# Kernel optimization log

Measured on AMD Instinct MI355X. Metric: run time of the kernel, lower is better.

Reference implementation:

```python
import jax, jax.numpy as jnp
import numpy as np

B, NP, DIM = 32, 1369, 768
NCLS, K = 200, 5
C = NCLS + 1          # n_classes + background
H = W = 37            # sqrt(NP)
GAMMA = 0.99
SCALE = 4.0
SINKHORN_ITERS = 3
PCA_ITERS = 10
PCA_THRESH = 0.5
EPS = 1e-8


def _l2norm(x):
    return x / jnp.clip(jnp.linalg.norm(x, axis=-1, keepdims=True), EPS)


def setup_inputs() -> dict:
    key = jax.random.key(0)
    k1, k2, k3 = jax.random.split(key, 3)
    patch_tokens = jax.random.normal(k1, (B, NP, DIM), dtype=jnp.float32)
    labels = jax.random.randint(k2, (B,), 0, NCLS)
    prototypes = 0.02 * jax.random.normal(k3, (C, K, DIM), dtype=jnp.float32)  # trunc_normal std=0.02 approx
    sa = jnp.full((NCLS, K), 0.5, dtype=jnp.float32)
    scale = jnp.asarray(SCALE, dtype=jnp.float32)
    return {"patch_tokens": patch_tokens, "labels": labels,
            "prototypes": prototypes, "sa": sa, "scale": scale}


def reference(patch_tokens, labels, prototypes, sa, scale):
    # --- cosine patch-prototype similarity ---
    tok_n = _l2norm(patch_tokens)                 # [B, NP, D]
    pro_n = _l2norm(prototypes)                   # [C, K, D]
    logits = scale * jnp.einsum('bnd,ckd->bnck', tok_n, pro_n)  # [B, NP, C, K]

    # --- avg pooling + 'sa' classification head ---
    image_logits = logits.mean(axis=1)            # [B, C, K]
    sa_w = jax.nn.softmax(sa, axis=-1) * K        # [NCLS, K]
    class_logits = (image_logits[:, :NCLS, :] * sa_w).sum(axis=-1)  # [B, NCLS]

    # --- PCA pseudo patch labels (power iteration, q=1, centered) ---
    X = jax.lax.stop_gradient(patch_tokens).reshape(-1, DIM)  # [N, D]
    Xc = X - X.mean(axis=0, keepdims=True)
    v = jax.random.normal(jax.random.key(42), (DIM,), dtype=jnp.float32)
    for _ in range(PCA_ITERS):
        u = Xc @ v
        v = Xc.T @ u
        v = v / jnp.clip(jnp.linalg.norm(v), EPS)
    u = Xc @ v
    U = u / jnp.clip(jnp.linalg.norm(u), EPS)     # leading left singular vector
    U_scaled = (U - U.min()) / jnp.clip(U.max() - U.min(), EPS)
    U_img = U_scaled.reshape(B, H, W)
    pseudo = jnp.where(U_img <= PCA_THRESH,
                       labels[:, None, None],
                       C - 1).astype(jnp.int32)   # [B, H, W]

    # --- online clustering: masked sinkhorn vectorized over classes ---
    flat_lab = pseudo.reshape(-1)                 # [N]
    cls_ids = jnp.arange(C)
    mask = (flat_lab[:, None] == cls_ids[None, :]).astype(jnp.float32)  # [N, C]
    Nc = mask.sum(axis=0)                         # [C] fg patch count per class
    Lf = jax.lax.stop_gradient(logits).reshape(-1, C, K)
    Q = jnp.exp(Lf) * mask[:, :, None]            # [N, C, K], zero outside class mask
    Q = Q / jnp.clip(Q.sum(axis=(0, 2)), EPS)[None, :, None]
    Ncc = jnp.clip(Nc, 1.0)
    for _ in range(SINKHORN_ITERS):
        Q = Q / jnp.clip(Q.sum(axis=0), EPS)[None] / K           # col normalize
        Q = Q / jnp.clip(Q.sum(axis=2, keepdims=True), EPS) / Ncc[None, :, None]  # row normalize
    Q = Q * Nc[None, :, None]
    tok_flat = jax.lax.stop_gradient(tok_n).reshape(-1, DIM)
    P_new = jnp.einsum('nck,nd->ckd', Q, tok_flat)               # [C, K, D]
    updated = GAMMA * prototypes + (1.0 - GAMMA) * P_new          # momentum update
    present = jnp.isin(cls_ids, labels)                           # classes in this batch
    new_prototypes = jnp.where(present[:, None, None], updated, prototypes)

    return (logits, image_logits, class_logits, pseudo, new_prototypes)
```

## Files before the change

### kernel.cpp

```cpp
#include <hip/hip_runtime.h>

constexpr int   BB    = 32;
constexpr int   NPP   = 1369;
constexpr int   DIMC  = 768;
constexpr int   NCLSC = 200;
constexpr int   KP    = 5;
constexpr int   CC    = 201;
constexpr int   CKC   = 1005;
constexpr int   NPAD  = 1024;
constexpr int   NTOK  = BB * NPP;
constexpr float EPSF  = 1e-8f;
constexpr int   PWIN  = 128;
constexpr int   MTILES = 343;
constexpr int   LDK   = 40;

typedef __attribute__((ext_vector_type(8))) short bf16x8;
typedef __attribute__((ext_vector_type(4))) float f32x4;

constexpr size_t O_LOG = 0;
constexpr size_t O_IMG = (size_t)NTOK * CKC;
constexpr size_t O_CLS = O_IMG + (size_t)BB * CKC;
constexpr size_t O_PSE = O_CLS + (size_t)BB * NCLSC;
constexpr size_t O_PRO = O_PSE + (size_t)NTOK;

constexpr size_t W_PRONBF = 0;
constexpr size_t W_INVN   = W_PRONBF + (size_t)NPAD*DIMC/2;
constexpr size_t W_MU     = W_INVN + NTOK;
constexpr size_t W_COLS   = W_MU + 2*DIMC;
constexpr size_t W_VBUF   = W_COLS + 2*DIMC;
constexpr size_t W_SSUM   = W_VBUF + 2*11*DIMC;
constexpr size_t W_TSUM   = W_SSUM + 32;
constexpr size_t W_NC     = W_TSUM + CC;
constexpr size_t W_FILL   = W_NC + CC;
constexpr size_t W_PRES   = W_FILL + CC;
constexpr size_t ZG_LEN   = (W_PRES + CC) - W_COLS;
constexpr size_t W_CSQ    = W_PRES + CC;
constexpr size_t W_U      = ((W_CSQ + CKC) + 1) & ~(size_t)1;
constexpr size_t W_PART   = W_U + 2*NTOK;
constexpr size_t W_SCAL   = W_PART + 2*1536;
constexpr size_t W_Q      = W_SCAL + 16;
constexpr size_t W_PNEW   = W_Q + (size_t)NTOK*KP;
constexpr size_t W_PLAB   = W_PNEW + (size_t)CC*KP*DIMC;
constexpr size_t W_OFFS   = W_PLAB + NTOK;
constexpr size_t W_RLST   = W_OFFS + 256;
constexpr size_t W_XBF    = ((W_RLST + NTOK) + 3) & ~(size_t)3;
constexpr size_t W_END_BIG  = W_XBF + (size_t)(NTOK + 128)*DIMC/2;
constexpr size_t W_PRON32   = W_XBF;
constexpr size_t W_END_FALL = W_PRON32 + (size_t)CKC*DIMC;

__device__ __forceinline__ unsigned short f2bf(float x) {
    unsigned u = __float_as_uint(x);
    unsigned r = (u + 0x7fffu + ((u >> 16) & 1u)) >> 16;
    return (unsigned short)r;
}

__global__ void fill_zero(float* p, int n) {
    int i = blockIdx.x * 256 + threadIdx.x;
    if (i < n) p[i] = 0.0f;
}

__global__ __launch_bounds__(256) void tok_stats(const float* __restrict__ X,
                                                 float* __restrict__ invn,
                                                 double* __restrict__ colsD,
                                                 unsigned short* __restrict__ xbf) {
    const int lane = threadIdx.x & 63;
    const int gw   = blockIdx.x * 4 + (threadIdx.x >> 6);
    double cacc[12];
    #pragma unroll
    for (int j = 0; j < 12; j++) cacc[j] = 0.0;
    for (int n = gw; n < NTOK; n += 1024) {
        const float* row = X + (size_t)n * DIMC;
        float s = 0.0f;
        float x[12];
        #pragma unroll
        for (int j = 0; j < 12; j++) {
            x[j] = row[lane + 64*j];
            s = fmaf(x[j], x[j], s);
            cacc[j] += (double)x[j];
        }
        if (xbf) {
            unsigned short* orow = xbf + (size_t)n * DIMC;
            #pragma unroll
            for (int j = 0; j < 12; j++) orow[lane + 64*j] = f2bf(x[j]);
        }
        #pragma unroll
        for (int o = 32; o >= 1; o >>= 1) s += __shfl_xor(s, o);
        if (lane == 0) invn[n] = 1.0f / fmaxf(sqrtf(s), EPSF);
    }
    #pragma unroll
    for (int j = 0; j < 12; j++) atomicAdd(&colsD[lane + 64*j], cacc[j]);
}

__global__ __launch_bounds__(256) void proto_norm(const float* __restrict__ P,
                                                  unsigned short* __restrict__ pbf,
                                                  float* __restrict__ p32) {
    const int lane = threadIdx.x & 63;
    const int gw   = blockIdx.x * 4 + (threadIdx.x >> 6);
    for (int j = gw; j < NPAD; j += 256) {
        unsigned short* obf = pbf + (size_t)j * DIMC;
        if (j >= CKC) {
            #pragma unroll
            for (int t = 0; t < 12; t++) obf[lane + 64*t] = 0;
            continue;
        }
        const float* row = P + (size_t)j * DIMC;
        float x[12]; float s = 0.0f;
        #pragma unroll
        for (int t = 0; t < 12; t++) { x[t] = row[lane + 64*t]; s = fmaf(x[t], x[t], s); }
        #pragma unroll
        for (int o = 32; o >= 1; o >>= 1) s += __shfl_xor(s, o);
        float nrm = fmaxf(sqrtf(s), EPSF);
        #pragma unroll
        for (int t = 0; t < 12; t++) {
            float nv = x[t] / nrm;
            obf[lane + 64*t] = f2bf(nv);
            if (p32) p32[(size_t)j * DIMC + lane + 64*t] = nv;
        }
    }
}

__global__ __launch_bounds__(256) void logits_gemm(
        const unsigned short* __restrict__ Xbf,
        const unsigned short* __restrict__ Pbf,
        const float* __restrict__ invn,
        const float* __restrict__ scale_p,
        float* __restrict__ out,
        float* __restrict__ img) {
    __shared__ unsigned short As[128 * LDK];
    __shared__ unsigned short Bs[128 * LDK];
    const int b   = blockIdx.x;
    const int swz = (b & 7) * MTILES + (b >> 3);
    const int row_t = swz >> 3, col_t = swz & 7;
    const int row0 = row_t * 128, col0 = col_t * 128;
    const int tid = threadIdx.x, lane = tid & 63, wid = tid >> 6;
    const int wm = (wid >> 1) * 64, wn = (wid & 1) * 64;
    const int fr = lane & 15, fq = lane >> 4;

    f32x4 acc[4][4] = {};

    const int srow = tid >> 1, sk = (tid & 1) * 16;
    const unsigned short* aSrc = Xbf + (size_t)(row0 + srow) * DIMC + sk;
    const unsigned short* bSrc = Pbf + (size_t)(col0 + srow) * DIMC + sk;
    unsigned short* aDst = As + srow * LDK + sk;
    unsigned short* bDst = Bs + srow * LDK + sk;

    for (int ks = 0; ks < DIMC / 32; ks++) {
        bf16x8 a0 = *(const bf16x8*)(aSrc + ks * 32);
        bf16x8 a1 = *(const bf16x8*)(aSrc + ks * 32 + 8);
        bf16x8 b0 = *(const bf16x8*)(bSrc + ks * 32);
        bf16x8 b1 = *(const bf16x8*)(bSrc + ks * 32 + 8);
        __syncthreads();
        *(bf16x8*)(aDst)     = a0; *(bf16x8*)(aDst + 8) = a1;
        *(bf16x8*)(bDst)     = b0; *(bf16x8*)(bDst + 8) = b1;
        __syncthreads();
        bf16x8 af[4], bfr[4];
        #pragma unroll
        for (int m = 0; m < 4; m++)
            af[m] = *(const bf16x8*)(As + (wm + m * 16 + fr) * LDK + fq * 8);
        #pragma unroll
        for (int n = 0; n < 4; n++)
            bfr[n] = *(const bf16x8*)(Bs + (wn + n * 16 + fr) * LDK + fq * 8);
        #pragma unroll
        for (int m = 0; m < 4; m++)
            #pragma unroll
            for (int n = 0; n < 4; n++)
                acc[m][n] = __builtin_amdgcn_mfma_f32_16x16x32_bf16(af[m], bfr[n], acc[m][n], 0, 0, 0);
    }

    const float sc = *scale_p;
    #pragma unroll
    for (int m = 0; m < 4; m++) {
        const int rbase = row0 + wm + m * 16 + fq * 4;
        float fin[4];
        #pragma unroll
        for (int rr = 0; rr < 4; rr++) {
            int rrow = rbase + rr;
            fin[rr] = (rrow < NTOK) ? sc * invn[rrow] : 0.0f;
        }
        const int strip0 = row0 + wm + m * 16;
        const bool sameImg = ((strip0 / NPP) == ((strip0 + 15) / NPP)) && (strip0 + 15) < NTOK;
        const int bimg = strip0 / NPP;
        #pragma unroll
        for (int n = 0; n < 4; n++) {
            const int col = col0 + wn + n * 16 + fr;
            const bool cok = col < CKC;
            float csum = 0.0f;
            #pragma unroll
            for (int rr = 0; rr < 4; rr++) {
                int rrow = rbase + rr;
                float v = fin[rr] * acc[m][n][rr];
                if (cok && rrow < NTOK) out[(size_t)rrow * CKC + col] = v;
                csum += v;
            }
            if (sameImg) {
                csum += __shfl_xor(csum, 16);
                csum += __shfl_xor(csum, 32);
                if (lane < 16 && cok) atomicAdd(&img[bimg * CKC + col], csum);
            } else if (cok) {
                #pragma unroll
                for (int rr = 0; rr < 4; rr++) {
                    int rrow = rbase + rr;
                    if (rrow < NTOK)
                        atomicAdd(&img[(rrow / NPP) * CKC + col], fin[rr] * acc[m][n][rr]);
                }
            }
        }
    }
}

__global__ __launch_bounds__(256) void gemm_logits(const float* __restrict__ X,
                                                   const float* __restrict__ Bn,
                                                   const float* __restrict__ invn,
                                                   const float* __restrict__ scale_p,
                                                   float* __restrict__ out) {
    __shared__ float As[32][68];
    __shared__ float Bs[32][68];
    const int tid = threadIdx.x;
    const int tx = tid & 15, ty = tid >> 4;
    const int row0 = blockIdx.x * 64;
    const int col0 = blockIdx.y * 64;
    const int lm = tid >> 2;
    const int kb = (tid & 3) * 8;
    float acc[4][4] = {};
    for (int k0 = 0; k0 < DIMC; k0 += 32) {
        float a[8], b[8];
        int ar = row0 + lm;
        if (ar < NTOK) {
            const float* ap = X + (size_t)ar * DIMC + k0 + kb;
            #pragma unroll
            for (int j = 0; j < 8; j++) a[j] = ap[j];
        } else {
            #pragma unroll
            for (int j = 0; j < 8; j++) a[j] = 0.0f;
        }
        int bc = col0 + lm;
        if (bc < CKC) {
            const float* bp = Bn + (size_t)bc * DIMC + k0 + kb;
            #pragma unroll
            for (int j = 0; j < 8; j++) b[j] = bp[j];
        } else {
            #pragma unroll
            for (int j = 0; j < 8; j++) b[j] = 0.0f;
        }
        __syncthreads();
        #pragma unroll
        for (int j = 0; j < 8; j++) As[kb + j][lm] = a[j];
        #pragma unroll
        for (int j = 0; j < 8; j++) Bs[kb + j][lm] = b[j];
        __syncthreads();
        #pragma unroll
        for (int kk = 0; kk < 32; kk++) {
            float av[4], bv[4];
            #pragma unroll
            for (int i = 0; i < 4; i++) av[i] = As[kk][ty*4 + i];
            #pragma unroll
            for (int j = 0; j < 4; j++) bv[j] = Bs[kk][tx*4 + j];
            #pragma unroll
            for (int i = 0; i < 4; i++)
                #pragma unroll
                for (int j = 0; j < 4; j++)
                    acc[i][j] = fmaf(av[i], bv[j], acc[i][j]);
        }
    }
    const float sc = *scale_p;
    #pragma unroll
    for (int i = 0; i < 4; i++) {
        int r = row0 + ty*4 + i;
        if (r >= NTOK) continue;
        float f = sc * invn[r];
        float* orow = out + (size_t)r * CKC;
        #pragma unroll
        for (int j = 0; j < 4; j++) {
            int c = col0 + tx*4 + j;
            if (c < CKC) orow[c] = f * acc[i][j];
        }
    }
}

__global__ void img_reduce(const float* __restrict__ logits, float* __restrict__ img) {
    int b = blockIdx.x, jc = blockIdx.y, nc = blockIdx.z;
    int j = jc * 256 + threadIdx.x;
    if (j >= CKC) return;
    int p0 = nc * 172, p1 = min(NPP, p0 + 172);
    const float* base = logits + (size_t)b * NPP * CKC + j;
    float s = 0.0f;
    for (int p = p0; p < p1; p++) s += base[(size_t)p * CKC];
    atomicAdd(&img[b * CKC + j], s);
}

__global__ __launch_bounds__(256) void img_final(float* __restrict__ img,
                                                 const float* __restrict__ sa,
                                                 float* __restrict__ cls) {
    int b = blockIdx.x;
    for (int i = threadIdx.x; i < CKC; i += 256)
        img[b * CKC + i] = img[b * CKC + i] / 1369.0f;
    __syncthreads();
    for (int c = threadIdx.x; c < NCLSC; c += 256) {
        float vv[KP]; float mx = -3.4e38f;
        #pragma unroll
        for (int k = 0; k < KP; k++) { vv[k] = sa[c * KP + k]; mx = fmaxf(mx, vv[k]); }
        float e[KP]; float s = 0.0f;
        #pragma unroll
        for (int k = 0; k < KP; k++) { e[k] = expf(vv[k] - mx); s += e[k]; }
        float cl = 0.0f;
        #pragma unroll
        for (int k = 0; k < KP; k++) {
            float sw = e[k] / s * 5.0f;
            cl += img[b * CKC + c * KP + k] * sw;
        }
        cls[b * NCLSC + c] = cl;
    }
}

__global__ void mu_final(const double* __restrict__ colsD, double* __restrict__ mu) {
    int d = threadIdx.x;
    mu[d] = colsD[d] / (double)NTOK;
}

__device__ __forceinline__ float bits_to_normal(unsigned bits) {
    float f = __uint_as_float((bits >> 9) | 0x3f800000u) - 1.0f;
    const float lo = -0.99999994f;
    float u = f * 2.0f + lo;
    u = fmaxf(lo, u);
    float w = -log1pf(-u * u);
    float p;
    if (w < 5.0f) {
        w -= 2.5f;
        p = 2.81022636e-08f;
        p = fmaf(p, w, 3.43273939e-07f);
        p = fmaf(p, w, -3.5233877e-06f);
        p = fmaf(p, w, -4.39150654e-06f);
        p = fmaf(p, w, 0.00021858087f);
        p = fmaf(p, w, -0.00125372503f);
        p = fmaf(p, w, -0.00417768164f);
        p = fmaf(p, w, 0.246640727f);
        p = fmaf(p, w, 1.50140941f);
    } else {
        w = sqrtf(w) - 3.0f;
        p = -0.000200214257f;
        p = fmaf(p, w, 0.000100950558f);
        p = fmaf(p, w, 0.00134934322f);
        p = fmaf(p, w, -0.00367342844f);
        p = fmaf(p, w, 0.00573950773f);
        p = fmaf(p, w, -0.0076224613f);
        p = fmaf(p, w, 0.00943887047f);
        p = fmaf(p, w, 1.00167406f);
        p = fmaf(p, w, 2.83297682f);
    }
    return 1.41421356237f * (p * u);
}

#define TF_ROUND(r) { x0 += x1; x1 = (x1 << r) | (x1 >> (32 - r)); x1 ^= x0; }
__global__ void v0_gen(double* __restrict__ v) {
    int i = blockIdx.x * 256 + threadIdx.x;
    if (i >= DIMC) return;
    unsigned x0 = 0u, x1 = (unsigned)i;
    const unsigned k0 = 0u, k1 = 42u, k2 = k0 ^ k1 ^ 0x1BD11BDAu;
    x0 += k0; x1 += k1;
    TF_ROUND(13) TF_ROUND(15) TF_ROUND(26) TF_ROUND(6)
    x0 += k1; x1 += k2 + 1u;
    TF_ROUND(17) TF_ROUND(29) TF_ROUND(16) TF_ROUND(24)
    x0 += k2; x1 += k0 + 2u;
    TF_ROUND(13) TF_ROUND(15) TF_ROUND(26) TF_ROUND(6)
    x0 += k0; x1 += k1 + 3u;
    TF_ROUND(17) TF_ROUND(29) TF_ROUND(16) TF_ROUND(24)
    x0 += k1; x1 += k2 + 4u;
    TF_ROUND(13) TF_ROUND(15) TF_ROUND(26) TF_ROUND(6)
    x0 += k2; x1 += k0 + 5u;
    v[i] = (double)bits_to_normal(x0 ^ x1);
}

__global__ __launch_bounds__(256) void pca_pass(const float* __restrict__ X,
                                                const double* __restrict__ mu,
                                                const double* __restrict__ vraw,
                                                const double* __restrict__ Sin,
                                                double* __restrict__ vnext,
                                                double* __restrict__ Snext) {
    __shared__ double ve[768];
    __shared__ double red[256];
    __shared__ double wacc[4][768];
    const int tid = threadIdx.x, lane = tid & 63, wid = tid >> 6;
    const double S = *Sin;
    double mv = 0.0;
    for (int c = tid; c < 768; c += 256) {
        double x = vraw[c] - S * mu[c];
        ve[c] = x;
        mv += mu[c] * x;
    }
    red[tid] = mv; __syncthreads();
    for (int s = 128; s > 0; s >>= 1) { if (tid < s) red[tid] += red[tid + s]; __syncthreads(); }
    const double muv = red[0];
    for (int c = tid; c < 4 * 768; c += 256) ((double*)wacc)[c] = 0.0;
    __syncthreads();
    double acc[12] = {};
    double usum = 0.0;
    for (int n = blockIdx.x * 4 + wid; n < NTOK; n += 2048) {
        const float* row = X + (size_t)n * DIMC;
        float x[12];
        double s = 0.0;
        #pragma unroll
        for (int j = 0; j < 12; j++) {
            x[j] = row[lane + 64*j];
            s = fma((double)x[j], ve[lane + 64*j], s);
        }
        #pragma unroll
        for (int o = 32; o >= 1; o >>= 1) s += __shfl_xor(s, o);
        double uu = s - muv;
        usum += uu;
        #pragma unroll
        for (int j = 0; j < 12; j++) acc[j] = fma((double)x[j], uu, acc[j]);
    }
    #pragma unroll
    for (int j = 0; j < 12; j++) wacc[wid][lane + 64*j] = acc[j];
    if (lane == 0) red[wid] = usum;
    __syncthreads();
    for (int c = tid; c < 768; c += 256)
        atomicAdd(&vnext[c], wacc[0][c] + wacc[1][c] + wacc[2][c] + wacc[3][c]);
    if (tid == 0) atomicAdd(Snext, red[0] + red[1] + red[2] + red[3]);
}

__global__ __launch_bounds__(256) void u_final(const float* __restrict__ X,
                                               const double* __restrict__ mu,
                                               const double* __restrict__ vraw,
                                               const double* __restrict__ Sin,
                                               double* __restrict__ u,
                                               double* __restrict__ part) {
    __shared__ double ve[768];
    __shared__ double red[256];
    __shared__ double wmin[4], wmax[4], wss[4];
    const int tid = threadIdx.x, lane = tid & 63, wid = tid >> 6;
    const double S = *Sin;
    double mv = 0.0;
    for (int c = tid; c < 768; c += 256) {
        double x = vraw[c] - S * mu[c];
        ve[c] = x;
        mv += mu[c] * x;
    }
    red[tid] = mv; __syncthreads();
    for (int s = 128; s > 0; s >>= 1) { if (tid < s) red[tid] += red[tid + s]; __syncthreads(); }
    const double muv = red[0];
    double lmin = 1e300, lmax = -1e300, lss = 0.0;
    for (int n = blockIdx.x * 4 + wid; n < NTOK; n += 2048) {
        const float* row = X + (size_t)n * DIMC;
        double s = 0.0;
        #pragma unroll
        for (int j = 0; j < 12; j++) s = fma((double)row[lane + 64*j], ve[lane + 64*j], s);
        #pragma unroll
        for (int o = 32; o >= 1; o >>= 1) s += __shfl_xor(s, o);
        double uu = s - muv;
        if (lane == 0) {
            u[n] = uu;
            lmin = fmin(lmin, uu); lmax = fmax(lmax, uu); lss = fma(uu, uu, lss);
        }
    }
    if (lane == 0) { wmin[wid] = lmin; wmax[wid] = lmax; wss[wid] = lss; }
    __syncthreads();
    if (tid == 0) {
        part[blockIdx.x]        = fmin(fmin(wmin[0], wmin[1]), fmin(wmin[2], wmin[3]));
        part[512 + blockIdx.x]  = fmax(fmax(wmax[0], wmax[1]), fmax(wmax[2], wmax[3]));
        part[1024 + blockIdx.x] = wss[0] + wss[1] + wss[2] + wss[3];
    }
}

__global__ __launch_bounds__(512) void final_scalars(const double* __restrict__ part,
                                                     double* __restrict__ scal,
                                                     const int* __restrict__ labels,
                                                     int* __restrict__ pres) {
    __shared__ double rmin[512], rmax[512], rss[512];
    int t = threadIdx.x;
    rmin[t] = part[t]; rmax[t] = part[512 + t]; rss[t] = part[1024 + t];
    __syncthreads();
    for (int s = 256; s > 0; s >>= 1) {
        if (t < s) {
            rmin[t] = fmin(rmin[t], rmin[t + s]);
            rmax[t] = fmax(rmax[t], rmax[t + s]);
            rss[t] += rss[t + s];
        }
        __syncthreads();
    }
    if (t == 0) {
        double nrm = fmax(sqrt(rss[0]), 1e-8);
        double Umin = rmin[0] / nrm;
        double Umax = rmax[0] / nrm;
        scal[1] = nrm;
        scal[2] = Umin;
        scal[3] = fmax(Umax - Umin, 1e-8);
    }
    if (t < BB) pres[labels[t]] = 1;
}

__global__ __launch_bounds__(256) void pseudo_kernel(
        const double* __restrict__ u, const double* __restrict__ scal,
        const int* __restrict__ labels, float* __restrict__ pse,
        int* __restrict__ plab, int* __restrict__ Nc) {
    __shared__ int hist[CC];
    const int tid = threadIdx.x;
    for (int c = tid; c < CC; c += 256) hist[c] = 0;
    __syncthreads();
    int n = blockIdx.x * 256 + tid;
    if (n < NTOK) {
        double U  = u[n] / scal[1];
        double Us = (U - scal[2]) / scal[3];
        int lab = (Us <= 0.5) ? labels[n / NPP] : (CC - 1);
        pse[n] = (float)lab;
        plab[n] = lab;
        atomicAdd(&hist[lab], 1);
    }
    __syncthreads();
    for (int c = tid; c < CC; c += 256)
        if (hist[c] > 0) atomicAdd(&Nc[c], hist[c]);
}

__global__ void offs_scan(const int* __restrict__ Nc, int* __restrict__ offs) {
    if (threadIdx.x == 0) {
        int s = 0;
        for (int c = 0; c < CC; c++) { offs[c] = s; s += Nc[c]; }
        offs[CC] = s;
    }
}

__global__ __launch_bounds__(256) void scatter_rows(
        const int* __restrict__ plab, const int* __restrict__ offs,
        int* __restrict__ fill, int* __restrict__ rlist) {
    __shared__ int hist[CC];
    __shared__ int base[CC];
    const int tid = threadIdx.x;
    for (int c = tid; c < CC; c += 256) hist[c] = 0;
    __syncthreads();
    int n = blockIdx.x * 256 + tid;
    int lab = -1, posl = 0;
    if (n < NTOK) {
        lab = plab[n];
        posl = atomicAdd(&hist[lab], 1);
    }
    __syncthreads();
    for (int c = tid; c < CC; c += 256) {
        int h = hist[c];
        if (h > 0) base[c] = atomicAdd(&fill[c], h);
    }
    __syncthreads();
    if (n < NTOK) rlist[offs[lab] + base[lab] + posl] = n;
}

__global__ __launch_bounds__(256) void sinkhorn_fused(
        const float* __restrict__ logits,
        const int* __restrict__ offs,
        const int* __restrict__ rlist,
        float* __restrict__ qseg) {
    const int c  = blockIdx.x;
    const int i0 = offs[c], i1 = offs[c + 1];
    const int cnt = i1 - i0;
    if (cnt <= 0) return;
    const int tid = threadIdx.x;
    __shared__ float cs[KP];
    __shared__ float redk[KP][4];

    for (int i = i0 + tid; i < i1; i += 256) {
        int n = rlist[i];
        const float* lp = logits + (size_t)n * CKC + c * KP;
        #pragma unroll
        for (int k = 0; k < KP; k++) qseg[(size_t)i * KP + k] = expf(lp[k]);
    }
    const float Ncc = fmaxf((float)cnt, 1.0f);
    for (int it = 0; it < 3; it++) {
        __syncthreads();
        float lc[KP] = {};
        for (int i = i0 + tid; i < i1; i += 256) {
            #pragma unroll
            for (int k = 0; k < KP; k++) lc[k] += qseg[(size_t)i * KP + k];
        }
        #pragma unroll
        for (int k = 0; k < KP; k++) {
            float v = lc[k];
            #pragma unroll
            for (int o = 32; o >= 1; o >>= 1) v += __shfl_xor(v, o);
            if ((tid & 63) == 0) redk[k][tid >> 6] = v;
        }
        __syncthreads();
        if (tid == 0) {
            #pragma unroll
            for (int k = 0; k < KP; k++)
                cs[k] = fmaxf(redk[k][0] + redk[k][1] + redk[k][2] + redk[k][3], EPSF) * 5.0f;
        }
        __syncthreads();
        float inv_cs[KP];
        #pragma unroll
        for (int k = 0; k < KP; k++) inv_cs[k] = 1.0f / cs[k];
        const float outsc = (it == 2) ? ((float)cnt / Ncc) : (1.0f / Ncc);
        for (int i = i0 + tid; i < i1; i += 256) {
            float v[KP]; float rs = 0.0f;
            #pragma unroll
            for (int k = 0; k < KP; k++) { v[k] = qseg[(size_t)i*KP + k] * inv_cs[k]; rs += v[k]; }
            float f = outsc / fmaxf(rs, EPSF);
            #pragma unroll
            for (int k = 0; k < KP; k++) qseg[(size_t)i*KP + k] = v[k] * f;
        }
    }
}

__global__ __launch_bounds__(256) void pnew_partial(
        const float* __restrict__ X,
        const float* __restrict__ invn,
        const float* __restrict__ qseg,
        const int* __restrict__ offs,
        const int* __restrict__ rlist,
        const int* __restrict__ plab,
        float* __restrict__ Pnew) {
    const int d = blockIdx.y * 256 + threadIdx.x;
    const int fgEnd = offs[CC - 1];
    int i0 = blockIdx.x * PWIN;
    if (i0 >= fgEnd) return;
    int i1 = min(i0 + PWIN, fgEnd);
    int curlab = -1;
    float acc[KP] = {};
    for (int i = i0; i < i1; i++) {
        int n = rlist[i];
        int lab = plab[n];
        if (lab != curlab) {
            if (curlab >= 0) {
                #pragma unroll
                for (int k = 0; k < KP; k++)
                    atomicAdd(&Pnew[((size_t)curlab * KP + k) * DIMC + d], acc[k]);
            }
            curlab = lab;
            #pragma unroll
            for (int k = 0; k < KP; k++) acc[k] = 0.0f;
        }
        float x = X[(size_t)n * DIMC + d] * invn[n];
        #pragma unroll
        for (int k = 0; k < KP; k++) acc[k] = fmaf(qseg[(size_t)i * KP + k], x, acc[k]);
    }
    if (curlab >= 0) {
        #pragma unroll
        for (int k = 0; k < KP; k++)
            atomicAdd(&Pnew[((size_t)curlab * KP + k) * DIMC + d], acc[k]);
    }
}

__global__ void proto_out(const float* __restrict__ proto, const float* __restrict__ Pnew,
                          const int* __restrict__ pres, float* __restrict__ outp) {
    int idx = blockIdx.x * 256 + threadIdx.x;
    if (idx >= CC * KP * DIMC) return;
    int c = idx / (KP * DIMC);
    float p = proto[idx];
    float r = p;
    if (pres[c]) {
        const float g = 0.99f;
        r = g * p + (1.0f - g) * Pnew[idx];
    }
    outp[idx] = r;
}

extern "C" void kernel_launch(void* const* d_in, const int* in_sizes, int n_in,
                              void* d_out, int out_size, void* d_ws, size_t ws_size,
                              hipStream_t stream) {
    const float* X      = (const float*)d_in[0];
    const int*   labels = (const int*)  d_in[1];
    const float* proto  = (const float*)d_in[2];
    const float* sa     = (const float*)d_in[3];
    const float* scale  = (const float*)d_in[4];
    float* out = (float*)d_out;
    float* ws  = (float*)d_ws;
    const bool big = ws_size >= W_END_BIG * sizeof(float);
    if (!big && ws_size < W_END_FALL * sizeof(float)) return;

    unsigned short* pronbf = (unsigned short*)(ws + W_PRONBF);
    float*  invn  = ws + W_INVN;
    double* mu    = (double*)(ws + W_MU);
    double* colsD = (double*)(ws + W_COLS);
    double* vbuf  = (double*)(ws + W_VBUF);
    double* Ssum  = (double*)(ws + W_SSUM);
    int*    Nc    = (int*)(ws + W_NC);
    int*    fill  = (int*)(ws + W_FILL);
    int*    pres  = (int*)(ws + W_PRES);
    double* u     = (double*)(ws + W_U);
    double* part  = (double*)(ws + W_PART);
    double* scal  = (double*)(ws + W_SCAL);
    float*  qseg  = ws + W_Q;
    float*  Pnew  = ws + W_PNEW;
    int*    plab  = (int*)(ws + W_PLAB);
    int*    offs  = (int*)(ws + W_OFFS);
    int*    rlist = (int*)(ws + W_RLST);
    unsigned short* xbf = big ? (unsigned short*)(ws + W_XBF) : nullptr;
    float*  pron32 = big ? nullptr : (ws + W_PRON32);

    fill_zero<<<((int)ZG_LEN + 255) / 256, 256, 0, stream>>>(ws + W_COLS, (int)ZG_LEN);
    fill_zero<<<(CC * KP * DIMC + 255) / 256, 256, 0, stream>>>(Pnew, CC * KP * DIMC);
    fill_zero<<<(BB * CKC + 255) / 256, 256, 0, stream>>>(out + O_IMG, BB * CKC);

    tok_stats<<<256, 256, 0, stream>>>(X, invn, colsD, xbf);
    proto_norm<<<64, 256, 0, stream>>>(proto, pronbf, pron32);
    if (big) {
        logits_gemm<<<MTILES * 8, 256, 0, stream>>>(xbf, pronbf, invn, scale,
                                                    out + O_LOG, out + O_IMG);
    } else {
        gemm_logits<<<dim3(685, 16), 256, 0, stream>>>(X, pron32, invn, scale, out + O_LOG);
        img_reduce<<<dim3(32, 4, 8), 256, 0, stream>>>(out + O_LOG, out + O_IMG);
    }
    img_final<<<32, 256, 0, stream>>>(out + O_IMG, sa, out + O_CLS);

    mu_final<<<1, 768, 0, stream>>>(colsD, mu);
    v0_gen<<<3, 256, 0, stream>>>(vbuf);
    for (int t = 0; t < 10; t++) {
        pca_pass<<<512, 256, 0, stream>>>(X, mu, vbuf + (size_t)t * DIMC, Ssum + t,
                                          vbuf + (size_t)(t + 1) * DIMC, Ssum + t + 1);
    }
    u_final<<<512, 256, 0, stream>>>(X, mu, vbuf + (size_t)10 * DIMC, Ssum + 10, u, part);
    final_scalars<<<1, 512, 0, stream>>>(part, scal, labels, pres);
    pseudo_kernel<<<172, 256, 0, stream>>>(u, scal, labels, out + O_PSE, plab, Nc);

    offs_scan<<<1, 64, 0, stream>>>(Nc, offs);
    scatter_rows<<<172, 256, 0, stream>>>(plab, offs, fill, rlist);
    sinkhorn_fused<<<NCLSC, 256, 0, stream>>>(out + O_LOG, offs, rlist, qseg);
    pnew_partial<<<dim3((NTOK + PWIN - 1) / PWIN, 3), 256, 0, stream>>>(
        X, invn, qseg, offs, rlist, plab, Pnew);
    proto_out<<<(CC * KP * DIMC + 255) / 256, 256, 0, stream>>>(proto, Pnew, pres, out + O_PRO);
}
```

Measured before the change: 714.0 us.

## Vectorize token loads, use direct global-to-LDS GEMM staging, widen PCA grid

Token statistics, the PCA power-iteration passes and the final projection now read rows as float4 and keep the centered direction vector in registers, which removes the shared-memory staging and the block tree reduction. The logits GEMM stages A and B tiles with global_load_lds 16-byte loads straight into unpadded LDS, so the register round trip goes away. The unpadded layout may bring LDS bank conflicts on fragment reads. The PCA pass grid doubles to 1024 blocks for more parallelism, at the cost of more atomic adds into the output vector.

```diff
diff --git a/kernel.cpp b/kernel.cpp
--- a/kernel.cpp
+++ b/kernel.cpp
@@ -12,7 +12,6 @@
 constexpr float EPSF  = 1e-8f;
 constexpr int   PWIN  = 128;
 constexpr int   MTILES = 343;
-constexpr int   LDK   = 40;
 
 typedef __attribute__((ext_vector_type(8))) short bf16x8;
 typedef __attribute__((ext_vector_type(4))) float f32x4;
@@ -54,6 +53,12 @@
     return (unsigned short)r;
 }
 
+typedef __attribute__((address_space(3))) unsigned int as3_u32;
+typedef __attribute__((address_space(1))) unsigned int as1_u32;
+__device__ __forceinline__ void gload16(const unsigned short* g, unsigned short* l) {
+    __builtin_amdgcn_global_load_lds((as1_u32*)g, (as3_u32*)l, 16, 0, 0);
+}
+
 __global__ void fill_zero(float* p, int n) {
     int i = blockIdx.x * 256 + threadIdx.x;
     if (i < n) p[i] = 0.0f;
@@ -65,30 +70,42 @@
                                                  unsigned short* __restrict__ xbf) {
     const int lane = threadIdx.x & 63;
     const int gw   = blockIdx.x * 4 + (threadIdx.x >> 6);
-    double cacc[12];
-    #pragma unroll
-    for (int j = 0; j < 12; j++) cacc[j] = 0.0;
+    double cacc[3][4];
+    #pragma unroll
+    for (int j = 0; j < 3; j++)
+        #pragma unroll
+        for (int t = 0; t < 4; t++) cacc[j][t] = 0.0;
     for (int n = gw; n < NTOK; n += 1024) {
-        const float* row = X + (size_t)n * DIMC;
+        const float4* row = (const float4*)(X + (size_t)n * DIMC);
         float s = 0.0f;
-        float x[12];
-        #pragma unroll
-        for (int j = 0; j < 12; j++) {
-            x[j] = row[lane + 64*j];
-            s = fmaf(x[j], x[j], s);
-            cacc[j] += (double)x[j];
+        float4 xv[3];
+        #pragma unroll
+        for (int j = 0; j < 3; j++) {
+            xv[j] = row[lane + 64*j];
+            s = fmaf(xv[j].x, xv[j].x, s); s = fmaf(xv[j].y, xv[j].y, s);
+            s = fmaf(xv[j].z, xv[j].z, s); s = fmaf(xv[j].w, xv[j].w, s);
+            cacc[j][0] += (double)xv[j].x; cacc[j][1] += (double)xv[j].y;
+            cacc[j][2] += (double)xv[j].z; cacc[j][3] += (double)xv[j].w;
         }
         if (xbf) {
             unsigned short* orow = xbf + (size_t)n * DIMC;
             #pragma unroll
-            for (int j = 0; j < 12; j++) orow[lane + 64*j] = f2bf(x[j]);
+            for (int j = 0; j < 3; j++) {
+                ushort4 pk;
+                pk.x = f2bf(xv[j].x); pk.y = f2bf(xv[j].y);
+                pk.z = f2bf(xv[j].z); pk.w = f2bf(xv[j].w);
+                *(ushort4*)(orow + 4*(lane + 64*j)) = pk;
+            }
         }
         #pragma unroll
         for (int o = 32; o >= 1; o >>= 1) s += __shfl_xor(s, o);
         if (lane == 0) invn[n] = 1.0f / fmaxf(sqrtf(s), EPSF);
     }
     #pragma unroll
-    for (int j = 0; j < 12; j++) atomicAdd(&colsD[lane + 64*j], cacc[j]);
+    for (int j = 0; j < 3; j++)
+        #pragma unroll
+        for (int t = 0; t < 4; t++)
+            atomicAdd(&colsD[4*lane + 256*j + t], cacc[j][t]);
 }
 
 __global__ __launch_bounds__(256) void proto_norm(const float* __restrict__ P,
@@ -126,8 +143,8 @@
         const float* __restrict__ scale_p,
         float* __restrict__ out,
         float* __restrict__ img) {
-    __shared__ unsigned short As[128 * LDK];
-    __shared__ unsigned short Bs[128 * LDK];
+    __shared__ unsigned short As[128 * 32];
+    __shared__ unsigned short Bs[128 * 32];
     const int b   = blockIdx.x;
     const int swz = (b & 7) * MTILES + (b >> 3);
     const int row_t = swz >> 3, col_t = swz & 7;
@@ -138,28 +155,31 @@
 
     f32x4 acc[4][4] = {};
 
-    const int srow = tid >> 1, sk = (tid & 1) * 16;
-    const unsigned short* aSrc = Xbf + (size_t)(row0 + srow) * DIMC + sk;
-    const unsigned short* bSrc = Pbf + (size_t)(col0 + srow) * DIMC + sk;
-    unsigned short* aDst = As + srow * LDK + sk;
-    unsigned short* bDst = Bs + srow * LDK + sk;
+    const int w32 = wid * 32;
+    const int lrow = lane >> 2, lk = (lane & 3) * 8;
+    const unsigned short* aS0 = Xbf + (size_t)(row0 + w32 + lrow) * DIMC + lk;
+    const unsigned short* aS1 = aS0 + (size_t)16 * DIMC;
+    const unsigned short* bS0 = Pbf + (size_t)(col0 + w32 + lrow) * DIMC + lk;
+    const unsigned short* bS1 = bS0 + (size_t)16 * DIMC;
+    unsigned short* aD0 = &As[(w32)      * 32];
+    unsigned short* aD1 = &As[(w32 + 16) * 32];
+    unsigned short* bD0 = &Bs[(w32)      * 32];
+    unsigned short* bD1 = &Bs[(w32 + 16) * 32];
 
     for (int ks = 0; ks < DIMC / 32; ks++) {
-        bf16x8 a0 = *(const bf16x8*)(aSrc + ks * 32);
-        bf16x8 a1 = *(const bf16x8*)(aSrc + ks * 32 + 8);
-        bf16x8 b0 = *(const bf16x8*)(bSrc + ks * 32);
-        bf16x8 b1 = *(const bf16x8*)(bSrc + ks * 32 + 8);
         __syncthreads();
-        *(bf16x8*)(aDst)     = a0; *(bf16x8*)(aDst + 8) = a1;
-        *(bf16x8*)(bDst)     = b0; *(bf16x8*)(bDst + 8) = b1;
+        gload16(aS0 + ks * 32, aD0);
+        gload16(aS1 + ks * 32, aD1);
+        gload16(bS0 + ks * 32, bD0);
+        gload16(bS1 + ks * 32, bD1);
         __syncthreads();
         bf16x8 af[4], bfr[4];
         #pragma unroll
         for (int m = 0; m < 4; m++)
-            af[m] = *(const bf16x8*)(As + (wm + m * 16 + fr) * LDK + fq * 8);
+            af[m] = *(const bf16x8*)(As + (wm + m * 16 + fr) * 32 + fq * 8);
         #pragma unroll
         for (int n = 0; n < 4; n++)
-            bfr[n] = *(const bf16x8*)(Bs + (wn + n * 16 + fr) * LDK + fq * 8);
+            bfr[n] = *(const bf16x8*)(Bs + (wn + n * 16 + fr) * 32 + fq * 8);
         #pragma unroll
         for (int m = 0; m < 4; m++)
             #pragma unroll
@@ -376,47 +396,62 @@
                                                 const double* __restrict__ Sin,
                                                 double* __restrict__ vnext,
                                                 double* __restrict__ Snext) {
-    __shared__ double ve[768];
-    __shared__ double red[256];
     __shared__ double wacc[4][768];
+    __shared__ double redw[4];
     const int tid = threadIdx.x, lane = tid & 63, wid = tid >> 6;
     const double S = *Sin;
+    double ver[3][4];
     double mv = 0.0;
-    for (int c = tid; c < 768; c += 256) {
-        double x = vraw[c] - S * mu[c];
-        ve[c] = x;
-        mv += mu[c] * x;
-    }
-    red[tid] = mv; __syncthreads();
-    for (int s = 128; s > 0; s >>= 1) { if (tid < s) red[tid] += red[tid + s]; __syncthreads(); }
-    const double muv = red[0];
-    for (int c = tid; c < 4 * 768; c += 256) ((double*)wacc)[c] = 0.0;
-    __syncthreads();
-    double acc[12] = {};
+    #pragma unroll
+    for (int j = 0; j < 3; j++)
+        #pragma unroll
+        for (int t = 0; t < 4; t++) {
+            int c = 4*lane + 256*j + t;
+            double x = vraw[c] - S * mu[c];
+            ver[j][t] = x;
+            mv += mu[c] * x;
+        }
+    #pragma unroll
+    for (int o = 32; o >= 1; o >>= 1) mv += __shfl_xor(mv, o);
+    const double muv = mv;
+
+    double acc[3][4] = {};
     double usum = 0.0;
-    for (int n = blockIdx.x * 4 + wid; n < NTOK; n += 2048) {
-        const float* row = X + (size_t)n * DIMC;
-        float x[12];
+    const int gw = blockIdx.x * 4 + wid;
+    for (int n = gw; n < NTOK; n += 4096) {
+        const float4* row = (const float4*)(X + (size_t)n * DIMC);
+        float4 xv[3];
         double s = 0.0;
         #pragma unroll
-        for (int j = 0; j < 12; j++) {
-            x[j] = row[lane + 64*j];
-            s = fma((double)x[j], ve[lane + 64*j], s);
+        for (int j = 0; j < 3; j++) {
+            xv[j] = row[lane + 64*j];
+            s = fma((double)xv[j].x, ver[j][0], s);
+            s = fma((double)xv[j].y, ver[j][1], s);
+            s = fma((double)xv[j].z, ver[j][2], s);
+            s = fma((double)xv[j].w, ver[j][3], s);
         }
         #pragma unroll
         for (int o = 32; o >= 1; o >>= 1) s += __shfl_xor(s, o);
         double uu = s - muv;
         usum += uu;
         #pragma unroll
-        for (int j = 0; j < 12; j++) acc[j] = fma((double)x[j], uu, acc[j]);
-    }
-    #pragma unroll
-    for (int j = 0; j < 12; j++) wacc[wid][lane + 64*j] = acc[j];
-    if (lane == 0) red[wid] = usum;
+        for (int j = 0; j < 3; j++) {
+            acc[j][0] = fma((double)xv[j].x, uu, acc[j][0]);
+            acc[j][1] = fma((double)xv[j].y, uu, acc[j][1]);
+            acc[j][2] = fma((double)xv[j].z, uu, acc[j][2]);
+            acc[j][3] = fma((double)xv[j].w, uu, acc[j][3]);
+        }
+    }
+    #pragma unroll
+    for (int j = 0; j < 3; j++)
+        #pragma unroll
+        for (int t = 0; t < 4; t++)
+            wacc[wid][4*lane + 256*j + t] = acc[j][t];
+    if (lane == 0) redw[wid] = usum;
     __syncthreads();
     for (int c = tid; c < 768; c += 256)
         atomicAdd(&vnext[c], wacc[0][c] + wacc[1][c] + wacc[2][c] + wacc[3][c]);
-    if (tid == 0) atomicAdd(Snext, red[0] + red[1] + red[2] + red[3]);
+    if (tid == 0) atomicAdd(Snext, redw[0] + redw[1] + redw[2] + redw[3]);
 }
 
 __global__ __launch_bounds__(256) void u_final(const float* __restrict__ X,
@@ -425,26 +460,35 @@
                                                const double* __restrict__ Sin,
                                                double* __restrict__ u,
                                                double* __restrict__ part) {
-    __shared__ double ve[768];
-    __shared__ double red[256];
     __shared__ double wmin[4], wmax[4], wss[4];
     const int tid = threadIdx.x, lane = tid & 63, wid = tid >> 6;
     const double S = *Sin;
+    double ver[3][4];
     double mv = 0.0;
-    for (int c = tid; c < 768; c += 256) {
-        double x = vraw[c] - S * mu[c];
-        ve[c] = x;
-        mv += mu[c] * x;
-    }
-    red[tid] = mv; __syncthreads();
-    for (int s = 128; s > 0; s >>= 1) { if (tid < s) red[tid] += red[tid + s]; __syncthreads(); }
-    const double muv = red[0];
+    #pragma unroll
+    for (int j = 0; j < 3; j++)
+        #pragma unroll
+        for (int t = 0; t < 4; t++) {
+            int c = 4*lane + 256*j + t;
+            double x = vraw[c] - S * mu[c];
+            ver[j][t] = x;
+            mv += mu[c] * x;
+        }
+    #pragma unroll
+    for (int o = 32; o >= 1; o >>= 1) mv += __shfl_xor(mv, o);
+    const double muv = mv;
     double lmin = 1e300, lmax = -1e300, lss = 0.0;
     for (int n = blockIdx.x * 4 + wid; n < NTOK; n += 2048) {
-        const float* row = X + (size_t)n * DIMC;
+        const float4* row = (const float4*)(X + (size_t)n * DIMC);
         double s = 0.0;
         #pragma unroll
-        for (int j = 0; j < 12; j++) s = fma((double)row[lane + 64*j], ve[lane + 64*j], s);
+        for (int j = 0; j < 3; j++) {
+            float4 xv = row[lane + 64*j];
+            s = fma((double)xv.x, ver[j][0], s);
+            s = fma((double)xv.y, ver[j][1], s);
+            s = fma((double)xv.z, ver[j][2], s);
+            s = fma((double)xv.w, ver[j][3], s);
+        }
         #pragma unroll
         for (int o = 32; o >= 1; o >>= 1) s += __shfl_xor(s, o);
         double uu = s - muv;
@@ -702,8 +746,8 @@
     mu_final<<<1, 768, 0, stream>>>(colsD, mu);
     v0_gen<<<3, 256, 0, stream>>>(vbuf);
     for (int t = 0; t < 10; t++) {
-        pca_pass<<<512, 256, 0, stream>>>(X, mu, vbuf + (size_t)t * DIMC, Ssum + t,
-                                          vbuf + (size_t)(t + 1) * DIMC, Ssum + t + 1);
+        pca_pass<<<1024, 256, 0, stream>>>(X, mu, vbuf + (size_t)t * DIMC, Ssum + t,
+                                           vbuf + (size_t)(t + 1) * DIMC, Ssum + t + 1);
     }
     u_final<<<512, 256, 0, stream>>>(X, mu, vbuf + (size_t)10 * DIMC, Ssum + 10, u, part);
     final_scalars<<<1, 512, 0, stream>>>(part, scal, labels, pres);
```

Result: slower. 833.2 us (+16.7%).
